# Performance work log

Measured on AMD Instinct MI355X. Metric: run time of the kernel, lower is better.

## Reference

```python
import jax, jax.numpy as jnp
import numpy as np

B, N, H, P, R = 16, 256, 768, 2048, 3


def setup_inputs() -> dict:
    key = jax.random.key(0)
    ks = jax.random.split(key, 7)
    s_h = 1.0 / np.sqrt(H)
    s_p = 1.0 / np.sqrt(P)
    return {
        "features": jax.random.normal(ks[0], (B, N, H), dtype=jnp.float32),
        "head_W": jax.random.uniform(ks[1], (P, H), jnp.float32, -s_h, s_h),
        "head_b": jax.random.uniform(ks[2], (P,), jnp.float32, -s_h, s_h),
        "tail_W": jax.random.uniform(ks[3], (P, H), jnp.float32, -s_h, s_h),
        "tail_b": jax.random.uniform(ks[4], (P,), jnp.float32, -s_h, s_h),
        "bil_W": jax.random.uniform(ks[5], (R, P, P), jnp.float32, -s_p, s_p),
        "bil_b": jax.random.uniform(ks[6], (R,), jnp.float32, -s_p, s_p),
    }


def reference(features, head_W, head_b, tail_W, tail_b, bil_W, bil_b):
    # Linear projections (dropout is identity in eval mode)
    head = jnp.einsum("bnh,ph->bnp", features, head_W) + head_b  # [B,N,P]
    tail = jnp.einsum("bnh,ph->bnp", features, tail_W) + tail_b  # [B,N,P]
    # Bilinear over all region pairs, without materializing [B,N,N,P]:
    # first contract head with W[r] -> [B,N,R,P], then with tail -> [B,N,N,R]
    hw = jnp.einsum("bnp,rpq->bnrq", head, bil_W)                # [B,N,R,P]
    logits = jnp.einsum("bnrq,bmq->bnmr", hw, tail) + bil_b      # [B,N,N,R]
    return logits
```

## Files before the change

kernel.cpp:

```cpp
#include <hip/hip_runtime.h>

constexpr int Bb = 16;
constexpr int Nn = 256;
constexpr int Hh = 768;
constexpr int Pp = 2048;
constexpr int Rr = 3;
constexpr int Mm = Bb * Nn;
constexpr int RQ = Rr * Pp;

typedef __bf16 bf16_t;
typedef __bf16 bf16x8 __attribute__((ext_vector_type(8)));
typedef __bf16 bf16x4 __attribute__((ext_vector_type(4)));
typedef float  floatx4 __attribute__((ext_vector_type(4)));

__device__ __forceinline__ void gld_lds16(const void* g, void* l) {
    __builtin_amdgcn_global_load_lds(
        (__attribute__((address_space(1))) void*)g,
        (__attribute__((address_space(3))) void*)l,
        16, 0, 0);
}

__global__ __launch_bounds__(256) void convert_kernel(
    const float* __restrict__ f, const float* __restrict__ tW,
    bf16_t* __restrict__ fo, bf16_t* __restrict__ tWo)
{
    const int i = blockIdx.x * 256 + threadIdx.x;
    if (i < Mm * Hh / 4) {
        float4 v = ((const float4*)f)[i];
        bf16x4 o = { (bf16_t)v.x, (bf16_t)v.y, (bf16_t)v.z, (bf16_t)v.w };
        *(bf16x4*)(fo + (size_t)i * 4) = o;
    }
    if (i < Pp * Hh / 4) {
        float4 w = ((const float4*)tW)[i];
        bf16x4 p = { (bf16_t)w.x, (bf16_t)w.y, (bf16_t)w.z, (bf16_t)w.w };
        *(bf16x4*)(tWo + (size_t)i * 4) = p;
    }
}

__global__ __launch_bounds__(256) void transpose_f32_bf16(
    const float* __restrict__ src, bf16_t* __restrict__ dst, int rows, int cols)
{
    __shared__ float t[32][33];
    const int r0 = blockIdx.y * 32;
    const int c0 = blockIdx.x * 32;
    const int tx = threadIdx.x, ty = threadIdx.y;
    #pragma unroll
    for (int s = 0; s < 4; ++s)
        t[ty + s * 8][tx] = src[(size_t)(r0 + ty + s * 8) * cols + c0 + tx];
    __syncthreads();
    #pragma unroll
    for (int s = 0; s < 4; ++s)
        dst[(size_t)(c0 + ty + s * 8) * rows + r0 + tx] = (bf16_t)t[tx][ty + s * 8];
}

__global__ __launch_bounds__(256) void transpose_bilW_kernel(
    const float* __restrict__ W, const float* __restrict__ bh,
    bf16_t* __restrict__ Wt, float* __restrict__ b2)
{
    __shared__ float t[32][33];
    const int r  = blockIdx.z;
    const int p0 = blockIdx.y * 32;
    const int q0 = blockIdx.x * 32;
    const int tx = threadIdx.x, ty = threadIdx.y;
    const float* src = W  + (size_t)r * Pp * Pp;
    bf16_t*      dst = Wt + (size_t)r * Pp * Pp;
    #pragma unroll
    for (int s = 0; s < 4; ++s)
        t[ty + s * 8][tx] = src[(size_t)(p0 + ty + s * 8) * Pp + q0 + tx];
    __syncthreads();
    #pragma unroll
    for (int s = 0; s < 4; ++s)
        dst[(size_t)(q0 + ty + s * 8) * Pp + p0 + tx] = (bf16_t)t[tx][ty + s * 8];
    if (ty == 0) {
        float s = 0.0f;
        #pragma unroll 8
        for (int pi = 0; pi < 32; ++pi)
            s += bh[p0 + pi] * t[pi][tx];
        atomicAdd(&b2[r * Pp + q0 + tx], s);
    }
}

template <int K, bool ADD_BIAS>
__global__ __launch_bounds__(256) void gemm_nt_128(
    const bf16_t* __restrict__ A,
    const bf16_t* __restrict__ B,
    const float*  __restrict__ bias,
    bf16_t* __restrict__ C, int ldc)
{
    __shared__ bf16_t As[128 * 32];
    __shared__ bf16_t Bs[128 * 32];

    const int tid = threadIdx.x;
    const int w = tid >> 6;
    const int l = tid & 63;
    const int m0 = blockIdx.y * 128;
    const int n0 = blockIdx.x * 128;

    const int srow = (w << 4) + (l >> 2);
    const int scol = (l & 3) << 3;
    const bf16_t* ga0 = A + (size_t)(m0 +      srow) * K + scol;
    const bf16_t* ga1 = A + (size_t)(m0 + 64 + srow) * K + scol;
    const bf16_t* gb0 = B + (size_t)(n0 +      srow) * K + scol;
    const bf16_t* gb1 = B + (size_t)(n0 + 64 + srow) * K + scol;
    char* la0 = (char*)As + (w << 10);
    char* la1 = (char*)As + 4096 + (w << 10);
    char* lb0 = (char*)Bs + (w << 10);
    char* lb1 = (char*)Bs + 4096 + (w << 10);

    const int wm = (w >> 1) << 6;
    const int wn = (w & 1) << 6;
    const int fr = l & 15;
    const int fq = (l >> 4) << 3;

    floatx4 acc[4][4] = {};

    for (int k0 = 0; k0 < K; k0 += 32) {
        __syncthreads();
        gld_lds16(ga0, la0); gld_lds16(ga1, la1);
        gld_lds16(gb0, lb0); gld_lds16(gb1, lb1);
        ga0 += 32; ga1 += 32; gb0 += 32; gb1 += 32;
        __syncthreads();

        bf16x8 a[4], b[4];
        #pragma unroll
        for (int i = 0; i < 4; ++i) {
            a[i] = *(const bf16x8*)&As[(wm + i * 16 + fr) * 32 + fq];
            b[i] = *(const bf16x8*)&Bs[(wn + i * 16 + fr) * 32 + fq];
        }
        #pragma unroll
        for (int i = 0; i < 4; ++i)
            #pragma unroll
            for (int j = 0; j < 4; ++j)
                acc[i][j] = __builtin_amdgcn_mfma_f32_16x16x32_bf16(a[i], b[j], acc[i][j], 0, 0, 0);
    }

    const int em = m0 + wm + ((l >> 4) << 2);
    const int en = n0 + wn + (l & 15);
    #pragma unroll
    for (int j = 0; j < 4; ++j) {
        const int n = en + j * 16;
        const float bv = ADD_BIAS ? bias[n] : 0.0f;
        #pragma unroll
        for (int i = 0; i < 4; ++i) {
            #pragma unroll
            for (int rg = 0; rg < 4; ++rg)
                C[(size_t)(em + i * 16 + rg) * ldc + n] = (bf16_t)(acc[i][j][rg] + bv);
        }
    }
}

__global__ __launch_bounds__(256) void gemm_out_fused(
    const bf16_t* __restrict__ HW,
    const bf16_t* __restrict__ TAIL,
    const float*  __restrict__ bil_b,
    float* __restrict__ OUT)
{
    __shared__ bf16_t S[2][4][64 * 32];

    const int b = blockIdx.z;
    const int n0 = blockIdx.y * 64;
    const int m0 = blockIdx.x * 64;

    const int tid = threadIdx.x;
    const int w = tid >> 6;
    const int l = tid & 63;

    const int srow = (w << 4) + (l >> 2);
    const int scol = (l & 3) << 3;

    const bf16_t* gh[Rr];
    #pragma unroll
    for (int r = 0; r < Rr; ++r)
        gh[r] = HW + (size_t)(b * Nn + n0 + srow) * RQ + r * Pp + scol;
    const bf16_t* gt = TAIL + (size_t)(b * Nn + m0 + srow) * Pp + scol;

    const int wn_ = (w >> 1) << 5;
    const int wm_ = (w & 1) << 5;
    const int fr = l & 15;
    const int fq = (l >> 4) << 3;

    floatx4 acc[Rr][2][2] = {};

    {
        char* base = (char*)&S[0][0][0] + (w << 10);
        #pragma unroll
        for (int r = 0; r < Rr; ++r) { gld_lds16(gh[r], base + r * 4096); gh[r] += 32; }
        gld_lds16(gt, base + 3 * 4096); gt += 32;
    }

    constexpr int STEPS = Pp / 32;
    for (int k = 0; k < STEPS; ++k) {
        __syncthreads();
        const int cur = k & 1;
        if (k + 1 < STEPS) {
            char* base = (char*)&S[cur ^ 1][0][0] + (w << 10);
            #pragma unroll
            for (int r = 0; r < Rr; ++r) { gld_lds16(gh[r], base + r * 4096); gh[r] += 32; }
            gld_lds16(gt, base + 3 * 4096); gt += 32;
        }

        bf16x8 t[2];
        #pragma unroll
        for (int j = 0; j < 2; ++j)
            t[j] = *(const bf16x8*)&S[cur][3][(wm_ + j * 16 + fr) * 32 + fq];
        #pragma unroll
        for (int r = 0; r < Rr; ++r) {
            bf16x8 a[2];
            #pragma unroll
            for (int i = 0; i < 2; ++i)
                a[i] = *(const bf16x8*)&S[cur][r][(wn_ + i * 16 + fr) * 32 + fq];
            #pragma unroll
            for (int i = 0; i < 2; ++i)
                #pragma unroll
                for (int j = 0; j < 2; ++j)
                    acc[r][i][j] = __builtin_amdgcn_mfma_f32_16x16x32_bf16(a[i], t[j], acc[r][i][j], 0, 0, 0);
        }
    }

    float bb[Rr] = { bil_b[0], bil_b[1], bil_b[2] };
    const int en_ = n0 + wn_ + ((l >> 4) << 2);
    const int em_ = m0 + wm_ + (l & 15);
    #pragma unroll
    for (int i = 0; i < 2; ++i)
        #pragma unroll
        for (int rg = 0; rg < 4; ++rg) {
            const int n = en_ + i * 16 + rg;
            #pragma unroll
            for (int j = 0; j < 2; ++j) {
                const int m = em_ + j * 16;
                float* o = OUT + (((size_t)b * Nn + n) * Nn + m) * Rr;
                #pragma unroll
                for (int r = 0; r < Rr; ++r)
                    o[r] = acc[r][i][j][rg] + bb[r];
            }
        }
}

extern "C" void kernel_launch(void* const* d_in, const int* in_sizes, int n_in,
                              void* d_out, int out_size, void* d_ws, size_t ws_size,
                              hipStream_t stream) {
    const float* features = (const float*)d_in[0];
    const float* head_W   = (const float*)d_in[1];
    const float* head_b   = (const float*)d_in[2];
    const float* tail_W   = (const float*)d_in[3];
    const float* tail_b   = (const float*)d_in[4];
    const float* bil_W    = (const float*)d_in[5];
    const float* bil_b    = (const float*)d_in[6];
    float* out = (float*)d_out;

    char* ws = (char*)d_ws;
    bf16_t* fbf     = (bf16_t*)ws;  ws += (size_t)Mm * Hh * 2;
    bf16_t* tWbf    = (bf16_t*)ws;  ws += (size_t)Pp * Hh * 2;
    bf16_t* hWT     = (bf16_t*)ws;  ws += (size_t)Hh * Pp * 2;
    bf16_t* W2T     = (bf16_t*)ws;  ws += (size_t)RQ * Hh * 2;
    float*  b2      = (float*)ws;   ws += (size_t)RQ * 4;
    bf16_t* tail_bf = (bf16_t*)ws;  ws += (size_t)Mm * Pp * 2;
    bf16_t* bilT    = (bf16_t*)ws;
    bf16_t* hw_all  = (bf16_t*)ws;  ws += (size_t)Mm * RQ * 2;

    hipMemsetAsync(b2, 0, (size_t)RQ * sizeof(float), stream);

    convert_kernel<<<Mm * Hh / 4 / 256, 256, 0, stream>>>(features, tail_W, fbf, tWbf);
    transpose_f32_bf16<<<dim3(Hh / 32, Pp / 32), dim3(32, 8), 0, stream>>>(
        head_W, hWT, Pp, Hh);
    transpose_bilW_kernel<<<dim3(Pp / 32, Pp / 32, Rr), dim3(32, 8), 0, stream>>>(
        bil_W, head_b, bilT, b2);

    gemm_nt_128<Hh, true><<<dim3(Pp / 128, Mm / 128), 256, 0, stream>>>(
        fbf, tWbf, tail_b, tail_bf, Pp);

    gemm_nt_128<Pp, false><<<dim3(Hh / 128, RQ / 128), 256, 0, stream>>>(
        bilT, hWT, nullptr, W2T, Hh);

    gemm_nt_128<Hh, true><<<dim3(RQ / 128, Mm / 128), 256, 0, stream>>>(
        fbf, W2T, b2, hw_all, RQ);

    gemm_out_fused<<<dim3(Nn / 64, Nn / 64, Bb), 256, 0, stream>>>(
        hw_all, tail_bf, bil_b, out);
}
```

Baseline: 276.8 us.

## Reassociate bilinear into H-space operator with augmented bias rows

Folds head_W, bil_W and tail_W into a per-relation H×H operator, with biases carried by an appended ones column. Features are then projected once into a 3×896 space, and the final pairwise GEMM contracts over K=896 instead of 2048. This removes the large Mm×RQ hw intermediate and the tail projection, and shrinks the dominant pair GEMM. In exchange it adds weight-side GEMMs (3×896×2048×2048 and 3×896×896×2080) and a full bf16 conversion of bil_W. It also rounds the composed operator to bf16, which may change numerics.

Result: slower. 290.6 us (+5.0%).

```diff
diff --git a/kernel.cpp b/kernel.cpp
--- a/kernel.cpp
+++ b/kernel.cpp
@@ -6,7 +6,9 @@
 constexpr int Pp = 2048;
 constexpr int Rr = 3;
 constexpr int Mm = Bb * Nn;
-constexpr int RQ = Rr * Pp;
+constexpr int HA = 896;
+constexpr int KA = 2080;
+constexpr int JA = Rr * HA;
 
 typedef __bf16 bf16_t;
 typedef __bf16 bf16x8 __attribute__((ext_vector_type(8)));
@@ -20,73 +22,99 @@
         16, 0, 0);
 }
 
-__global__ __launch_bounds__(256) void convert_kernel(
-    const float* __restrict__ f, const float* __restrict__ tW,
-    bf16_t* __restrict__ fo, bf16_t* __restrict__ tWo)
-{
-    const int i = blockIdx.x * 256 + threadIdx.x;
-    if (i < Mm * Hh / 4) {
-        float4 v = ((const float4*)f)[i];
-        bf16x4 o = { (bf16_t)v.x, (bf16_t)v.y, (bf16_t)v.z, (bf16_t)v.w };
-        *(bf16x4*)(fo + (size_t)i * 4) = o;
-    }
-    if (i < Pp * Hh / 4) {
-        float4 w = ((const float4*)tW)[i];
-        bf16x4 p = { (bf16_t)w.x, (bf16_t)w.y, (bf16_t)w.z, (bf16_t)w.w };
-        *(bf16x4*)(tWo + (size_t)i * 4) = p;
-    }
-}
-
-__global__ __launch_bounds__(256) void transpose_f32_bf16(
-    const float* __restrict__ src, bf16_t* __restrict__ dst, int rows, int cols)
+__global__ __launch_bounds__(256) void build_Faug(
+    const float* __restrict__ F, bf16_t* __restrict__ out)
+{
+    const int idx = blockIdx.x * 256 + threadIdx.x;
+    const int n = idx / (HA / 4), c4 = idx % (HA / 4);
+    const int h = c4 * 4;
+    bf16x4 o;
+    if (h < Hh) {
+        float4 v = *(const float4*)(F + (size_t)n * Hh + h);
+        o = { (bf16_t)v.x, (bf16_t)v.y, (bf16_t)v.z, (bf16_t)v.w };
+    } else {
+        #pragma unroll
+        for (int e = 0; e < 4; ++e) o[e] = (bf16_t)((h + e == Hh) ? 1.0f : 0.0f);
+    }
+    *(bf16x4*)(out + (size_t)n * HA + h) = o;
+}
+
+__global__ __launch_bounds__(256) void convert_bil(
+    const float* __restrict__ W, bf16_t* __restrict__ o)
+{
+    const size_t i = (size_t)blockIdx.x * 256 + threadIdx.x;
+    float4 v = ((const float4*)W)[i];
+    bf16x4 b = { (bf16_t)v.x, (bf16_t)v.y, (bf16_t)v.z, (bf16_t)v.w };
+    *(bf16x4*)(o + i * 4) = b;
+}
+
+__global__ __launch_bounds__(256) void build_tWaug(
+    const float* __restrict__ tW, const float* __restrict__ bt,
+    bf16_t* __restrict__ out)
 {
     __shared__ float t[32][33];
-    const int r0 = blockIdx.y * 32;
-    const int c0 = blockIdx.x * 32;
+    const int j0 = blockIdx.y * 32, q0 = blockIdx.x * 32;
     const int tx = threadIdx.x, ty = threadIdx.y;
     #pragma unroll
-    for (int s = 0; s < 4; ++s)
-        t[ty + s * 8][tx] = src[(size_t)(r0 + ty + s * 8) * cols + c0 + tx];
+    for (int s = 0; s < 4; ++s) {
+        const int q = q0 + ty + s * 8, j = j0 + tx;
+        t[ty + s * 8][tx] = (j < Hh) ? tW[(size_t)q * Hh + j] : 0.0f;
+    }
     __syncthreads();
     #pragma unroll
-    for (int s = 0; s < 4; ++s)
-        dst[(size_t)(c0 + ty + s * 8) * rows + r0 + tx] = (bf16_t)t[tx][ty + s * 8];
-}
-
-__global__ __launch_bounds__(256) void transpose_bilW_kernel(
-    const float* __restrict__ W, const float* __restrict__ bh,
-    bf16_t* __restrict__ Wt, float* __restrict__ b2)
+    for (int s = 0; s < 4; ++s) {
+        const int j = j0 + ty + s * 8, q = q0 + tx;
+        float v = t[tx][ty + s * 8];
+        if (j == Hh) v = bt[q];
+        else if (j > Hh) v = 0.0f;
+        out[(size_t)j * Pp + q] = (bf16_t)v;
+    }
+}
+
+__global__ __launch_bounds__(256) void build_hWaug(
+    const float* __restrict__ hW, const float* __restrict__ bh,
+    bf16_t* __restrict__ out)
 {
     __shared__ float t[32][33];
-    const int r  = blockIdx.z;
-    const int p0 = blockIdx.y * 32;
-    const int q0 = blockIdx.x * 32;
+    const int h0 = blockIdx.y * 32, p0 = blockIdx.x * 32;
     const int tx = threadIdx.x, ty = threadIdx.y;
-    const float* src = W  + (size_t)r * Pp * Pp;
-    bf16_t*      dst = Wt + (size_t)r * Pp * Pp;
-    #pragma unroll
-    for (int s = 0; s < 4; ++s)
-        t[ty + s * 8][tx] = src[(size_t)(p0 + ty + s * 8) * Pp + q0 + tx];
+    #pragma unroll
+    for (int s = 0; s < 4; ++s) {
+        const int p = p0 + ty + s * 8, h = h0 + tx;
+        t[ty + s * 8][tx] = (p < Pp && h < Hh) ? hW[(size_t)p * Hh + h] : 0.0f;
+    }
     __syncthreads();
     #pragma unroll
-    for (int s = 0; s < 4; ++s)
-        dst[(size_t)(q0 + ty + s * 8) * Pp + p0 + tx] = (bf16_t)t[tx][ty + s * 8];
-    if (ty == 0) {
-        float s = 0.0f;
-        #pragma unroll 8
-        for (int pi = 0; pi < 32; ++pi)
-            s += bh[p0 + pi] * t[pi][tx];
-        atomicAdd(&b2[r * Pp + q0 + tx], s);
-    }
-}
-
-template <int K, bool ADD_BIAS>
+    for (int s = 0; s < 4; ++s) {
+        const int h = h0 + ty + s * 8, p = p0 + tx;
+        float v = t[tx][ty + s * 8];
+        if (h == Hh) v = (p < Pp) ? bh[p] : (p == Pp ? 1.0f : 0.0f);
+        else if (h > Hh) v = 0.0f;
+        out[(size_t)h * KA + p] = (bf16_t)v;
+    }
+}
+
+__global__ __launch_bounds__(256) void fill_T1cols(
+    const float* __restrict__ bil_b, bf16_t* __restrict__ T1)
+{
+    const int idx = blockIdx.x * 256 + threadIdx.x;
+    if (idx >= Rr * HA) return;
+    const int r = idx / HA, j = idx % HA;
+    bf16_t* p = T1 + (size_t)r * HA * KA + (size_t)j * KA + Pp;
+    p[0] = (bf16_t)(j == Hh ? bil_b[r] : 0.0f);
+    #pragma unroll
+    for (int e = 1; e < 32; ++e) p[e] = (bf16_t)0.0f;
+}
+
 __global__ __launch_bounds__(256) void gemm_nt_128(
-    const bf16_t* __restrict__ A,
-    const bf16_t* __restrict__ B,
-    const float*  __restrict__ bias,
-    bf16_t* __restrict__ C, int ldc)
-{
+    const bf16_t* __restrict__ A, int lda, size_t sA,
+    const bf16_t* __restrict__ B, int ldb, size_t sB,
+    bf16_t* __restrict__ C, int ldc, size_t sC, int K)
+{
+    A += (size_t)blockIdx.z * sA;
+    B += (size_t)blockIdx.z * sB;
+    C += (size_t)blockIdx.z * sC;
+
     __shared__ bf16_t As[128 * 32];
     __shared__ bf16_t Bs[128 * 32];
 
@@ -98,10 +126,10 @@
 
     const int srow = (w << 4) + (l >> 2);
     const int scol = (l & 3) << 3;
-    const bf16_t* ga0 = A + (size_t)(m0 +      srow) * K + scol;
-    const bf16_t* ga1 = A + (size_t)(m0 + 64 + srow) * K + scol;
-    const bf16_t* gb0 = B + (size_t)(n0 +      srow) * K + scol;
-    const bf16_t* gb1 = B + (size_t)(n0 + 64 + srow) * K + scol;
+    const bf16_t* ga0 = A + (size_t)(m0 +      srow) * lda + scol;
+    const bf16_t* ga1 = A + (size_t)(m0 + 64 + srow) * lda + scol;
+    const bf16_t* gb0 = B + (size_t)(n0 +      srow) * ldb + scol;
+    const bf16_t* gb1 = B + (size_t)(n0 + 64 + srow) * ldb + scol;
     char* la0 = (char*)As + (w << 10);
     char* la1 = (char*)As + 4096 + (w << 10);
     char* lb0 = (char*)Bs + (w << 10);
@@ -139,20 +167,18 @@
     #pragma unroll
     for (int j = 0; j < 4; ++j) {
         const int n = en + j * 16;
-        const float bv = ADD_BIAS ? bias[n] : 0.0f;
         #pragma unroll
         for (int i = 0; i < 4; ++i) {
             #pragma unroll
             for (int rg = 0; rg < 4; ++rg)
-                C[(size_t)(em + i * 16 + rg) * ldc + n] = (bf16_t)(acc[i][j][rg] + bv);
+                C[(size_t)(em + i * 16 + rg) * ldc + n] = (bf16_t)(acc[i][j][rg]);
         }
     }
 }
 
 __global__ __launch_bounds__(256) void gemm_out_fused(
-    const bf16_t* __restrict__ HW,
-    const bf16_t* __restrict__ TAIL,
-    const float*  __restrict__ bil_b,
+    const bf16_t* __restrict__ FG,
+    const bf16_t* __restrict__ FA,
     float* __restrict__ OUT)
 {
     __shared__ bf16_t S[2][4][64 * 32];
@@ -171,8 +197,8 @@
     const bf16_t* gh[Rr];
     #pragma unroll
     for (int r = 0; r < Rr; ++r)
-        gh[r] = HW + (size_t)(b * Nn + n0 + srow) * RQ + r * Pp + scol;
-    const bf16_t* gt = TAIL + (size_t)(b * Nn + m0 + srow) * Pp + scol;
+        gh[r] = FG + (size_t)(b * Nn + n0 + srow) * JA + r * HA + scol;
+    const bf16_t* gt = FA + (size_t)(b * Nn + m0 + srow) * HA + scol;
 
     const int wn_ = (w >> 1) << 5;
     const int wm_ = (w & 1) << 5;
@@ -188,7 +214,7 @@
         gld_lds16(gt, base + 3 * 4096); gt += 32;
     }
 
-    constexpr int STEPS = Pp / 32;
+    constexpr int STEPS = HA / 32;
     for (int k = 0; k < STEPS; ++k) {
         __syncthreads();
         const int cur = k & 1;
@@ -217,7 +243,6 @@
         }
     }
 
-    float bb[Rr] = { bil_b[0], bil_b[1], bil_b[2] };
     const int en_ = n0 + wn_ + ((l >> 4) << 2);
     const int em_ = m0 + wm_ + (l & 15);
     #pragma unroll
@@ -231,7 +256,7 @@
                 float* o = OUT + (((size_t)b * Nn + n) * Nn + m) * Rr;
                 #pragma unroll
                 for (int r = 0; r < Rr; ++r)
-                    o[r] = acc[r][i][j][rg] + bb[r];
+                    o[r] = acc[r][i][j][rg];
             }
         }
 }
@@ -249,32 +274,34 @@
     float* out = (float*)d_out;
 
     char* ws = (char*)d_ws;
-    bf16_t* fbf     = (bf16_t*)ws;  ws += (size_t)Mm * Hh * 2;
-    bf16_t* tWbf    = (bf16_t*)ws;  ws += (size_t)Pp * Hh * 2;
-    bf16_t* hWT     = (bf16_t*)ws;  ws += (size_t)Hh * Pp * 2;
-    bf16_t* W2T     = (bf16_t*)ws;  ws += (size_t)RQ * Hh * 2;
-    float*  b2      = (float*)ws;   ws += (size_t)RQ * 4;
-    bf16_t* tail_bf = (bf16_t*)ws;  ws += (size_t)Mm * Pp * 2;
-    bf16_t* bilT    = (bf16_t*)ws;
-    bf16_t* hw_all  = (bf16_t*)ws;  ws += (size_t)Mm * RQ * 2;
-
-    hipMemsetAsync(b2, 0, (size_t)RQ * sizeof(float), stream);
-
-    convert_kernel<<<Mm * Hh / 4 / 256, 256, 0, stream>>>(features, tail_W, fbf, tWbf);
-    transpose_f32_bf16<<<dim3(Hh / 32, Pp / 32), dim3(32, 8), 0, stream>>>(
-        head_W, hWT, Pp, Hh);
-    transpose_bilW_kernel<<<dim3(Pp / 32, Pp / 32, Rr), dim3(32, 8), 0, stream>>>(
-        bil_W, head_b, bilT, b2);
-
-    gemm_nt_128<Hh, true><<<dim3(Pp / 128, Mm / 128), 256, 0, stream>>>(
-        fbf, tWbf, tail_b, tail_bf, Pp);
-
-    gemm_nt_128<Pp, false><<<dim3(Hh / 128, RQ / 128), 256, 0, stream>>>(
-        bilT, hWT, nullptr, W2T, Hh);
-
-    gemm_nt_128<Hh, true><<<dim3(RQ / 128, Mm / 128), 256, 0, stream>>>(
-        fbf, W2T, b2, hw_all, RQ);
-
-    gemm_out_fused<<<dim3(Nn / 64, Nn / 64, Bb), 256, 0, stream>>>(
-        hw_all, tail_bf, bil_b, out);
-}
+    bf16_t* Faug   = (bf16_t*)ws;  ws += (size_t)Mm * HA * 2;
+    bf16_t* bilbf  = (bf16_t*)ws;  ws += (size_t)Rr * Pp * Pp * 2;
+    bf16_t* tWaug  = (bf16_t*)ws;  ws += (size_t)HA * Pp * 2;
+    bf16_t* hWaug  = (bf16_t*)ws;  ws += (size_t)HA * KA * 2;
+    bf16_t* T1taug = (bf16_t*)ws;  ws += (size_t)Rr * HA * KA * 2;
+    bf16_t* Bop    = (bf16_t*)ws;  ws += (size_t)Rr * HA * HA * 2;
+    bf16_t* FG     = (bf16_t*)ws;  ws += (size_t)Mm * JA * 2;
+
+    build_Faug<<<Mm * (HA / 4) / 256, 256, 0, stream>>>(features, Faug);
+    convert_bil<<<(int)((size_t)Rr * Pp * Pp / 4 / 256), 256, 0, stream>>>(bil_W, bilbf);
+    build_tWaug<<<dim3(Pp / 32, HA / 32), dim3(32, 8), 0, stream>>>(tail_W, tail_b, tWaug);
+    build_hWaug<<<dim3(KA / 32, HA / 32), dim3(32, 8), 0, stream>>>(head_W, head_b, hWaug);
+
+    gemm_nt_128<<<dim3(Pp / 128, HA / 128, Rr), 256, 0, stream>>>(
+        tWaug, Pp, 0,
+        bilbf, Pp, (size_t)Pp * Pp,
+        T1taug, KA, (size_t)HA * KA, Pp);
+    fill_T1cols<<<(Rr * HA + 255) / 256, 256, 0, stream>>>(bil_b, T1taug);
+
+    gemm_nt_128<<<dim3(HA / 128, HA / 128, Rr), 256, 0, stream>>>(
+        T1taug, KA, (size_t)HA * KA,
+        hWaug, KA, 0,
+        Bop, HA, (size_t)HA * HA, KA);
+
+    gemm_nt_128<<<dim3(JA / 128, Mm / 128, 1), 256, 0, stream>>>(
+        Faug, HA, 0,
+        Bop, HA, 0,
+        FG, JA, 0, HA);
+
+    gemm_out_fused<<<dim3(Nn / 64, Nn / 64, Bb), 256, 0, stream>>>(FG, Faug, out);
+}
```
